# Performance work log

Hardware: AMD Instinct MI355X
Metric: run time of the kernel (lower is better)

Reference implementation:

```python
import math
import jax, jax.numpy as jnp
import numpy as np

SQRT_2_OVER_PI = 0.7978845608028654
FACIL_RATE = 2.0
FIRE_THRESH = 0.88
EPS = 1e-05

def _gelu(x):
    return 0.5 * x * (1.0 + jnp.tanh(SQRT_2_OVER_PI * (x + 0.044715 * x ** 3)))

def setup_inputs() -> dict:
    key = jax.random.key(0)
    ks = jax.random.split(key, 8)
    B, T, D, N = 4, 4096, 1024, 512
    x = jax.random.normal(ks[0], (B, T, D), jnp.float32)
    ema_x = jax.random.normal(ks[1], (D,), jnp.float32) * 0.1
    ema_x2 = ema_x ** 2 + jax.random.uniform(ks[2], (D,), jnp.float32) + 0.5
    ema_y = jax.random.normal(ks[3], (D,), jnp.float32) * 0.1
    ema_y2 = ema_y ** 2 + jax.random.uniform(ks[4], (D,), jnp.float32) + 0.5
    buf = jax.random.normal(ks[5], (N, D), jnp.float32)
    buf = buf / jnp.linalg.norm(buf, axis=-1, keepdims=True)
    facil = 1.0 + 2.0 * jax.random.uniform(ks[6], (N,), jnp.float32)  # facilitation levels >= 1
    mask = jnp.ones((N,), dtype=bool)
    return {
        'x': x,
        'log_tau_in': jnp.float32(math.log(1.0)),
        'log_tau_out': jnp.float32(math.log(1.0)),
        'log_a_in': jnp.float32(0.0),
        'log_a_out': jnp.float32(0.0),
        'log_k_boost': jnp.float32(math.log(0.5)),
        'log_k_damp': jnp.float32(math.log(0.3)),
        'ema_x': ema_x, 'ema_x2': ema_x2, 'ema_y': ema_y, 'ema_y2': ema_y2,
        'buf': buf, 'facil': facil, 'mask': mask,
    }

def reference(x, log_tau_in, log_tau_out, log_a_in, log_a_out,
              log_k_boost, log_k_damp, ema_x, ema_x2, ema_y, ema_y2,
              buf, facil, mask):
    sg = jax.lax.stop_gradient
    D = x.shape[-1]
    y = _gelu(x)
    # --- gate_211 (l1_ready steady state); z-statistics are detached in torch ---
    tau_in, tau_out = jnp.exp(log_tau_in), jnp.exp(log_tau_out)
    a_in, a_out = jax.nn.sigmoid(log_a_in), jax.nn.sigmoid(log_a_out)
    std_x = jnp.sqrt(jnp.clip(sg(ema_x2) - sg(ema_x) ** 2, 0.0)) + EPS
    z_in = jnp.mean(((sg(x) - sg(ema_x)) / std_x) ** 2, axis=-1)        # [B,T]
    std_y = jnp.sqrt(jnp.clip(sg(ema_y2) - sg(ema_y) ** 2, 0.0)) + EPS
    z_out = jnp.mean(((sg(y) - sg(ema_y)) / std_y) ** 2, axis=-1)       # [B,T]
    g_in = 1.0 - a_in + a_in * jnp.exp(-tau_in * z_in)
    g_out = 1.0 - a_out + a_out * jnp.exp(-tau_out * z_out)
    gate = g_in * g_out
    y1 = y * gate[..., None]
    # --- eval-time OCS nearest-neighbor facilitation (l2_ready, pass1_complete) ---
    k_boost = jnp.clip(jnp.exp(log_k_boost), 0.01, 4.0)
    k_damp = jnp.clip(jnp.exp(log_k_damp), 0.01, 0.9)
    y1_mean = jnp.mean(sg(y1).reshape(-1, D), axis=0)                    # [D]
    m_n = y1_mean / jnp.maximum(jnp.linalg.norm(y1_mean), 1e-12)
    buf_sg = sg(buf)
    buf_n = buf_sg / jnp.maximum(jnp.linalg.norm(buf_sg, axis=-1, keepdims=True), 1e-12)
    sims = jnp.where(mask, buf_n @ m_n, -1.0)                            # [N]
    nearest_idx = jnp.argmax(sims)
    sim_val = jnp.clip(sims[nearest_idx], 0.0, 1.0)
    fired = sim_val > FIRE_THRESH
    facil_level = sg(facil)[nearest_idx] * jnp.where(fired, FACIL_RATE, 1.0)
    v = buf_sg[nearest_idx]                                              # [D]
    valid = jnp.all(jnp.isfinite(v)) & (jnp.linalg.norm(v) >= 1e-06)
    mod = (facil_level - 1.0) * sim_val
    boost = 1.0 + sg(k_boost) * mod            # torch uses .item(): detached
    damp = jnp.maximum(0.01, 1.0 - sg(k_damp) * mod)
    proj = jnp.sum(y1 * v, axis=-1, keepdims=True)
    y_par = proj * v
    out = jnp.where(valid, y_par * boost + (y1 - y_par) * damp, y1)
    return out
```

## Files before the change

### kernel.cpp

```cpp
#include <hip/hip_runtime.h>
#include <math.h>

#define D 1024
#define NROWS 16384
#define NBUF 512

#define OFF_MEAN 0
#define OFF_KEY  1024
#define OFF_GATE 2048
#define OFF_PART 20480
#define ZERO_BYTES 4112

typedef float nfloat4 __attribute__((ext_vector_type(4)));

__device__ __forceinline__ float4 ld4(const float* p) { return *(const float4*)p; }
__device__ __forceinline__ void st4_nt(float* p, float4 v) {
    nfloat4 nv = { v.x, v.y, v.z, v.w };
    __builtin_nontemporal_store(nv, (nfloat4*)p);
}

__device__ __forceinline__ float wave_red(float v) {
    #pragma unroll
    for (int off = 32; off > 0; off >>= 1) v += __shfl_xor(v, off, 64);
    return v;
}

__device__ __forceinline__ float gelu_f(float x) {
    float u = 0.7978845608028654f * (x + 0.044715f * x * x * x);
    float e = __expf(2.0f * u);
    float t = 1.0f - 2.0f / (e + 1.0f);
    return 0.5f * x * (1.0f + t);
}

__device__ __forceinline__ float4 inv_std4(float4 m, float4 m2) {
    float4 r;
    r.x = 1.0f / (sqrtf(fmaxf(m2.x - m.x * m.x, 0.f)) + 1e-5f);
    r.y = 1.0f / (sqrtf(fmaxf(m2.y - m.y * m.y, 0.f)) + 1e-5f);
    r.z = 1.0f / (sqrtf(fmaxf(m2.z - m.z * m.z, 0.f)) + 1e-5f);
    r.w = 1.0f / (sqrtf(fmaxf(m2.w - m.w * m.w, 0.f)) + 1e-5f);
    return r;
}

template<int RPW>
__global__ __launch_bounds__(256, 4) void k_passA(const float* __restrict__ x,
                                                  const float* __restrict__ ema_x,
                                                  const float* __restrict__ ema_x2,
                                                  const float* __restrict__ ema_y,
                                                  const float* __restrict__ ema_y2,
                                                  const float* __restrict__ lti,
                                                  const float* __restrict__ lto,
                                                  const float* __restrict__ lai,
                                                  const float* __restrict__ lao,
                                                  float* __restrict__ ws) {
    __shared__ float s_acc[D];
    const int tid = threadIdx.x;
    const int wave = tid >> 6, lane = tid & 63;
    for (int i = tid; i < D; i += 256) s_acc[i] = 0.0f;
    __syncthreads();

    const float tau_in = __expf(lti[0]), tau_out = __expf(lto[0]);
    const float a_in  = 1.0f / (1.0f + __expf(-lai[0]));
    const float a_out = 1.0f / (1.0f + __expf(-lao[0]));

    int col[4];
    float4 emx[4], isx[4], emy[4], isy[4];
    #pragma unroll
    for (int j = 0; j < 4; ++j) {
        col[j] = 4 * lane + 256 * j;
        emx[j] = ld4(&ema_x[col[j]]);
        isx[j] = inv_std4(emx[j], ld4(&ema_x2[col[j]]));
        emy[j] = ld4(&ema_y[col[j]]);
        isy[j] = inv_std4(emy[j], ld4(&ema_y2[col[j]]));
    }
    float4 acc[4];
    #pragma unroll
    for (int j = 0; j < 4; ++j) acc[j] = make_float4(0.f, 0.f, 0.f, 0.f);

    const int r0 = (blockIdx.x * 4 + wave) * RPW;
    for (int r = r0; r < r0 + RPW; ++r) {
        const float* xr = x + (size_t)r * D;
        float4 yv[4];
        float zin = 0.f, zout = 0.f;
        #pragma unroll
        for (int j = 0; j < 4; ++j) {
            float4 xv = ld4(&xr[col[j]]);
            float dx, dy;
            dx = (xv.x - emx[j].x) * isx[j].x; zin += dx * dx;
            dx = (xv.y - emx[j].y) * isx[j].y; zin += dx * dx;
            dx = (xv.z - emx[j].z) * isx[j].z; zin += dx * dx;
            dx = (xv.w - emx[j].w) * isx[j].w; zin += dx * dx;
            yv[j].x = gelu_f(xv.x); dy = (yv[j].x - emy[j].x) * isy[j].x; zout += dy * dy;
            yv[j].y = gelu_f(xv.y); dy = (yv[j].y - emy[j].y) * isy[j].y; zout += dy * dy;
            yv[j].z = gelu_f(xv.z); dy = (yv[j].z - emy[j].z) * isy[j].z; zout += dy * dy;
            yv[j].w = gelu_f(xv.w); dy = (yv[j].w - emy[j].w) * isy[j].w; zout += dy * dy;
        }
        zin  = wave_red(zin)  * (1.0f / D);
        zout = wave_red(zout) * (1.0f / D);
        float g = ((1.0f - a_in)  + a_in  * __expf(-tau_in  * zin)) *
                  ((1.0f - a_out) + a_out * __expf(-tau_out * zout));
        if (lane == 0) ws[OFF_GATE + r] = g;
        #pragma unroll
        for (int j = 0; j < 4; ++j) {
            acc[j].x += yv[j].x * g;
            acc[j].y += yv[j].y * g;
            acc[j].z += yv[j].z * g;
            acc[j].w += yv[j].w * g;
        }
    }
    #pragma unroll
    for (int j = 0; j < 4; ++j) {
        atomicAdd(&s_acc[col[j] + 0], acc[j].x);
        atomicAdd(&s_acc[col[j] + 1], acc[j].y);
        atomicAdd(&s_acc[col[j] + 2], acc[j].z);
        atomicAdd(&s_acc[col[j] + 3], acc[j].w);
    }
    __syncthreads();
    float4 pv = *(float4*)&s_acc[tid * 4];
    *(float4*)&ws[OFF_PART + (size_t)blockIdx.x * D + tid * 4] = pv;
}

__global__ __launch_bounds__(256) void k_mean(float* __restrict__ ws) {
    const int tid = threadIdx.x;
    const float* P = &ws[OFF_PART + (size_t)blockIdx.x * 16 * D];
    float4 s = make_float4(0.f, 0.f, 0.f, 0.f);
    #pragma unroll
    for (int i = 0; i < 16; ++i) {
        float4 v = ld4(&P[(size_t)i * D + 4 * tid]);
        s.x += v.x; s.y += v.y; s.z += v.z; s.w += v.w;
    }
    atomicAdd(&ws[OFF_MEAN + 4 * tid + 0], s.x);
    atomicAdd(&ws[OFF_MEAN + 4 * tid + 1], s.y);
    atomicAdd(&ws[OFF_MEAN + 4 * tid + 2], s.z);
    atomicAdd(&ws[OFF_MEAN + 4 * tid + 3], s.w);
}

__global__ __launch_bounds__(256) void k_sims(const float* __restrict__ buf,
                                              const unsigned char* __restrict__ mask,
                                              float* __restrict__ ws) {
    __shared__ float s_red[4];
    __shared__ float s_inv;
    const int tid = threadIdx.x, wave = tid >> 6, lane = tid & 63;

    float4 mv = ld4(&ws[OFF_MEAN + tid * 4]);
    float ns = mv.x * mv.x + mv.y * mv.y + mv.z * mv.z + mv.w * mv.w;
    ns = wave_red(ns);
    if (lane == 0) s_red[wave] = ns;
    __syncthreads();
    if (tid == 0) {
        float t = s_red[0] + s_red[1] + s_red[2] + s_red[3];
        s_inv = 1.0f / fmaxf(sqrtf(t), 1e-12f);
    }
    __syncthreads();
    const float inv = s_inv;

    int col[4];
    float4 mvv[4];
    #pragma unroll
    for (int j = 0; j < 4; ++j) {
        col[j] = 4 * lane + 256 * j;
        mvv[j] = ld4(&ws[OFF_MEAN + col[j]]);
    }
    const int n = blockIdx.x * 4 + wave;
    const float* br = buf + (size_t)n * D;
    float dot = 0.f, bns = 0.f;
    #pragma unroll
    for (int j = 0; j < 4; ++j) {
        float4 bv = ld4(&br[col[j]]);
        dot += bv.x * mvv[j].x + bv.y * mvv[j].y + bv.z * mvv[j].z + bv.w * mvv[j].w;
        bns += bv.x * bv.x + bv.y * bv.y + bv.z * bv.z + bv.w * bv.w;
    }
    dot = wave_red(dot);
    bns = wave_red(bns);
    if (lane == 0) {
        float sim = -1.0f;
        if (mask[n]) sim = (dot * inv) / fmaxf(sqrtf(bns), 1e-12f);
        unsigned int fb = __float_as_uint(sim);
        unsigned int mono = (fb & 0x80000000u) ? ~fb : (fb | 0x80000000u);
        unsigned long long key = ((unsigned long long)mono << 32) | (unsigned int)(~n);
        atomicMax((unsigned long long*)&ws[OFF_KEY], key);
    }
}

__global__ __launch_bounds__(256, 4) void k_passB(const float* __restrict__ x,
                                                  const float* __restrict__ buf,
                                                  const float* __restrict__ facil,
                                                  const float* __restrict__ lkb,
                                                  const float* __restrict__ lkd,
                                                  const float* __restrict__ ws,
                                                  float* __restrict__ out) {
    __shared__ float s_red[4];
    __shared__ float s_sc[3];
    const int tid = threadIdx.x, wave = tid >> 6, lane = tid & 63;

    const unsigned long long key = *(const unsigned long long*)&ws[OFF_KEY];
    const int idx = (int)(~(unsigned int)(key & 0xFFFFFFFFull));
    const unsigned int mono = (unsigned int)(key >> 32);
    const unsigned int fb = (mono & 0x80000000u) ? (mono ^ 0x80000000u) : ~mono;
    const float sim = __uint_as_float(fb);

    int col[4];
    float4 vv[4];
    const float* vrow = buf + (size_t)idx * D;
    float bns = 0.f;
    #pragma unroll
    for (int j = 0; j < 4; ++j) {
        col[j] = 4 * lane + 256 * j;
        vv[j] = ld4(&vrow[col[j]]);
        if (!isfinite(vv[j].x)) bns = __uint_as_float(0x7FC00000u);
        if (!isfinite(vv[j].y)) bns = __uint_as_float(0x7FC00000u);
        if (!isfinite(vv[j].z)) bns = __uint_as_float(0x7FC00000u);
        if (!isfinite(vv[j].w)) bns = __uint_as_float(0x7FC00000u);
        bns += vv[j].x * vv[j].x + vv[j].y * vv[j].y + vv[j].z * vv[j].z + vv[j].w * vv[j].w;
    }
    bns = wave_red(bns);
    if (lane == 0) s_red[wave] = bns;
    __syncthreads();
    if (tid == 0) {
        float t = s_red[0] + s_red[1] + s_red[2] + s_red[3];
        int valid = (t >= 1e-12f) ? 1 : 0;
        float sim_val = fminf(fmaxf(sim, 0.0f), 1.0f);
        float fl = facil[idx] * ((sim_val > 0.88f) ? 2.0f : 1.0f);
        float mod = (fl - 1.0f) * sim_val;
        float kb = fminf(fmaxf(__expf(lkb[0]), 0.01f), 4.0f);
        float kd = fminf(fmaxf(__expf(lkd[0]), 0.01f), 0.9f);
        float boost = 1.0f + kb * mod;
        float damp = fmaxf(0.01f, 1.0f - kd * mod);
        s_sc[0] = valid ? damp : 1.0f;
        s_sc[1] = valid ? (boost - damp) : 0.0f;
        s_sc[2] = (float)valid;
    }
    __syncthreads();
    const float dampe = s_sc[0], coef = s_sc[1];
    if (s_sc[2] == 0.0f) {
        #pragma unroll
        for (int j = 0; j < 4; ++j) vv[j] = make_float4(0.f, 0.f, 0.f, 0.f);
    }

    const int r0 = (blockIdx.x * 4 + wave) * 2;
    for (int r = r0; r < r0 + 2; ++r) {
        const float* xr = x + (size_t)r * D;
        const float g = ws[OFF_GATE + r];
        float4 y1[4];
        float proj = 0.f;
        #pragma unroll
        for (int j = 0; j < 4; ++j) {
            float4 xv = ld4(&xr[col[j]]);
            y1[j].x = gelu_f(xv.x) * g; proj += y1[j].x * vv[j].x;
            y1[j].y = gelu_f(xv.y) * g; proj += y1[j].y * vv[j].y;
            y1[j].z = gelu_f(xv.z) * g; proj += y1[j].z * vv[j].z;
            y1[j].w = gelu_f(xv.w) * g; proj += y1[j].w * vv[j].w;
        }
        proj = wave_red(proj);
        const float pc = proj * coef;
        float* orow = out + (size_t)r * D;
        #pragma unroll
        for (int j = 0; j < 4; ++j) {
            float4 o;
            o.x = y1[j].x * dampe + pc * vv[j].x;
            o.y = y1[j].y * dampe + pc * vv[j].y;
            o.z = y1[j].z * dampe + pc * vv[j].z;
            o.w = y1[j].w * dampe + pc * vv[j].w;
            st4_nt(&orow[col[j]], o);
        }
    }
}

extern "C" void kernel_launch(void* const* d_in, const int* in_sizes, int n_in,
                              void* d_out, int out_size, void* d_ws, size_t ws_size,
                              hipStream_t stream) {
    const float* x      = (const float*)d_in[0];
    const float* lti    = (const float*)d_in[1];
    const float* lto    = (const float*)d_in[2];
    const float* lai    = (const float*)d_in[3];
    const float* lao    = (const float*)d_in[4];
    const float* lkb    = (const float*)d_in[5];
    const float* lkd    = (const float*)d_in[6];
    const float* ema_x  = (const float*)d_in[7];
    const float* ema_x2 = (const float*)d_in[8];
    const float* ema_y  = (const float*)d_in[9];
    const float* ema_y2 = (const float*)d_in[10];
    const float* buf    = (const float*)d_in[11];
    const float* facil  = (const float*)d_in[12];
    const unsigned char* mask = (const unsigned char*)d_in[13];
    float* ws  = (float*)d_ws;
    float* out = (float*)d_out;

    int NP;
    if      (ws_size >= ((size_t)OFF_PART + 2048u * D) * 4) NP = 2048;
    else if (ws_size >= ((size_t)OFF_PART + 1024u * D) * 4) NP = 1024;
    else                                                    NP = 512;

    (void)hipMemsetAsync(d_ws, 0, ZERO_BYTES, stream);
    if (NP == 2048)
        hipLaunchKernelGGL(k_passA<2>, dim3(2048), dim3(256), 0, stream,
                           x, ema_x, ema_x2, ema_y, ema_y2, lti, lto, lai, lao, ws);
    else if (NP == 1024)
        hipLaunchKernelGGL(k_passA<4>, dim3(1024), dim3(256), 0, stream,
                           x, ema_x, ema_x2, ema_y, ema_y2, lti, lto, lai, lao, ws);
    else
        hipLaunchKernelGGL(k_passA<8>, dim3(512), dim3(256), 0, stream,
                           x, ema_x, ema_x2, ema_y, ema_y2, lti, lto, lai, lao, ws);
    hipLaunchKernelGGL(k_mean,  dim3(NP / 16), dim3(256), 0, stream, ws);
    hipLaunchKernelGGL(k_sims,  dim3(128), dim3(256), 0, stream, buf, mask, ws);
    hipLaunchKernelGGL(k_passB, dim3(2048), dim3(256), 0, stream,
                       x, buf, facil, lkb, lkd, ws, out);
}
```

Baseline: 217.8 us.

## Process two rows per iteration, fold stats into LDS, cheaper GELU, fewer blocks

Several changes land together. GELU is rewritten algebraically as x - x/(1+exp(2u)) using a hardware reciprocal. The EMA statistics are precomputed per block into shared memory as a scale and an offset so the z-scores become FMAs. Both passes now handle two rows per iteration with all loads issued up front, and each wave covers 8 rows. Grids are fixed at 512 blocks for pass A and pass B, dropping the workspace-size-dependent partial count. The aim is more memory-level parallelism and less ALU work, at the cost of more registers and fewer blocks in flight.

```diff
diff --git a/kernel.cpp b/kernel.cpp
--- a/kernel.cpp
+++ b/kernel.cpp
@@ -4,6 +4,7 @@
 #define D 1024
 #define NROWS 16384
 #define NBUF 512
+#define NBLKA 512
 
 #define OFF_MEAN 0
 #define OFF_KEY  1024
@@ -26,22 +27,20 @@
 }
 
 __device__ __forceinline__ float gelu_f(float x) {
-    float u = 0.7978845608028654f * (x + 0.044715f * x * x * x);
-    float e = __expf(2.0f * u);
-    float t = 1.0f - 2.0f / (e + 1.0f);
-    return 0.5f * x * (1.0f + t);
-}
-
-__device__ __forceinline__ float4 inv_std4(float4 m, float4 m2) {
-    float4 r;
-    r.x = 1.0f / (sqrtf(fmaxf(m2.x - m.x * m.x, 0.f)) + 1e-5f);
-    r.y = 1.0f / (sqrtf(fmaxf(m2.y - m.y * m.y, 0.f)) + 1e-5f);
-    r.z = 1.0f / (sqrtf(fmaxf(m2.z - m.z * m.z, 0.f)) + 1e-5f);
-    r.w = 1.0f / (sqrtf(fmaxf(m2.w - m.w * m.w, 0.f)) + 1e-5f);
-    return r;
-}
-
-template<int RPW>
+    float x2 = x * x;
+    float t1 = fmaf(0.044715f, x2, 1.0f);
+    float u2 = (1.5957691216057308f * x) * t1;
+    float e  = __expf(u2);
+    float r  = __builtin_amdgcn_rcpf(e + 1.0f);
+    return fmaf(-x, r, x);
+}
+
+__device__ __forceinline__ float4 gelu4(float4 x) {
+    float4 y;
+    y.x = gelu_f(x.x); y.y = gelu_f(x.y); y.z = gelu_f(x.z); y.w = gelu_f(x.w);
+    return y;
+}
+
 __global__ __launch_bounds__(256, 4) void k_passA(const float* __restrict__ x,
                                                   const float* __restrict__ ema_x,
                                                   const float* __restrict__ ema_x2,
@@ -52,10 +51,23 @@
                                                   const float* __restrict__ lai,
                                                   const float* __restrict__ lao,
                                                   float* __restrict__ ws) {
+    __shared__ float s_stat[4096];
     __shared__ float s_acc[D];
-    const int tid = threadIdx.x;
-    const int wave = tid >> 6, lane = tid & 63;
-    for (int i = tid; i < D; i += 256) s_acc[i] = 0.0f;
+    const int tid = threadIdx.x, wave = tid >> 6, lane = tid & 63;
+
+    for (int i = tid; i < 1024; i += 256) {
+        float mx = ema_x[i];
+        float vx = fmaxf(ema_x2[i] - mx * mx, 0.0f);
+        float ax = 1.0f / (sqrtf(vx) + 1e-5f);
+        s_stat[i]        = ax;
+        s_stat[1024 + i] = mx * ax;
+        float my = ema_y[i];
+        float vy = fmaxf(ema_y2[i] - my * my, 0.0f);
+        float ay = 1.0f / (sqrtf(vy) + 1e-5f);
+        s_stat[2048 + i] = ay;
+        s_stat[3072 + i] = my * ay;
+        s_acc[i] = 0.0f;
+    }
     __syncthreads();
 
     const float tau_in = __expf(lti[0]), tau_out = __expf(lto[0]);
@@ -63,48 +75,66 @@
     const float a_out = 1.0f / (1.0f + __expf(-lao[0]));
 
     int col[4];
-    float4 emx[4], isx[4], emy[4], isy[4];
-    #pragma unroll
-    for (int j = 0; j < 4; ++j) {
-        col[j] = 4 * lane + 256 * j;
-        emx[j] = ld4(&ema_x[col[j]]);
-        isx[j] = inv_std4(emx[j], ld4(&ema_x2[col[j]]));
-        emy[j] = ld4(&ema_y[col[j]]);
-        isy[j] = inv_std4(emy[j], ld4(&ema_y2[col[j]]));
-    }
+    #pragma unroll
+    for (int j = 0; j < 4; ++j) col[j] = 4 * lane + 256 * j;
+
     float4 acc[4];
     #pragma unroll
     for (int j = 0; j < 4; ++j) acc[j] = make_float4(0.f, 0.f, 0.f, 0.f);
 
-    const int r0 = (blockIdx.x * 4 + wave) * RPW;
-    for (int r = r0; r < r0 + RPW; ++r) {
-        const float* xr = x + (size_t)r * D;
-        float4 yv[4];
-        float zin = 0.f, zout = 0.f;
+    const int r0 = (blockIdx.x * 4 + wave) * 8;
+    #pragma unroll
+    for (int k = 0; k < 4; ++k) {
+        const int rA = r0 + 2 * k, rB = rA + 1;
+        const float* pA = x + (size_t)rA * D;
+        const float* pB = x + (size_t)rB * D;
+        float4 xA[4], xB[4];
+        #pragma unroll
+        for (int j = 0; j < 4; ++j) { xA[j] = ld4(&pA[col[j]]); xB[j] = ld4(&pB[col[j]]); }
+
+        float4 yA[4], yB[4];
+        float zinA = 0.f, zinB = 0.f, zoutA = 0.f, zoutB = 0.f;
         #pragma unroll
         for (int j = 0; j < 4; ++j) {
-            float4 xv = ld4(&xr[col[j]]);
-            float dx, dy;
-            dx = (xv.x - emx[j].x) * isx[j].x; zin += dx * dx;
-            dx = (xv.y - emx[j].y) * isx[j].y; zin += dx * dx;
-            dx = (xv.z - emx[j].z) * isx[j].z; zin += dx * dx;
-            dx = (xv.w - emx[j].w) * isx[j].w; zin += dx * dx;
-            yv[j].x = gelu_f(xv.x); dy = (yv[j].x - emy[j].x) * isy[j].x; zout += dy * dy;
-            yv[j].y = gelu_f(xv.y); dy = (yv[j].y - emy[j].y) * isy[j].y; zout += dy * dy;
-            yv[j].z = gelu_f(xv.z); dy = (yv[j].z - emy[j].z) * isy[j].z; zout += dy * dy;
-            yv[j].w = gelu_f(xv.w); dy = (yv[j].w - emy[j].w) * isy[j].w; zout += dy * dy;
+            float4 a  = *(const float4*)&s_stat[col[j]];
+            float4 bb = *(const float4*)&s_stat[1024 + col[j]];
+            float d;
+            d = fmaf(xA[j].x, a.x, -bb.x); zinA = fmaf(d, d, zinA);
+            d = fmaf(xA[j].y, a.y, -bb.y); zinA = fmaf(d, d, zinA);
+            d = fmaf(xA[j].z, a.z, -bb.z); zinA = fmaf(d, d, zinA);
+            d = fmaf(xA[j].w, a.w, -bb.w); zinA = fmaf(d, d, zinA);
+            d = fmaf(xB[j].x, a.x, -bb.x); zinB = fmaf(d, d, zinB);
+            d = fmaf(xB[j].y, a.y, -bb.y); zinB = fmaf(d, d, zinB);
+            d = fmaf(xB[j].z, a.z, -bb.z); zinB = fmaf(d, d, zinB);
+            d = fmaf(xB[j].w, a.w, -bb.w); zinB = fmaf(d, d, zinB);
+            yA[j] = gelu4(xA[j]);
+            yB[j] = gelu4(xB[j]);
+            float4 ay = *(const float4*)&s_stat[2048 + col[j]];
+            float4 by = *(const float4*)&s_stat[3072 + col[j]];
+            d = fmaf(yA[j].x, ay.x, -by.x); zoutA = fmaf(d, d, zoutA);
+            d = fmaf(yA[j].y, ay.y, -by.y); zoutA = fmaf(d, d, zoutA);
+            d = fmaf(yA[j].z, ay.z, -by.z); zoutA = fmaf(d, d, zoutA);
+            d = fmaf(yA[j].w, ay.w, -by.w); zoutA = fmaf(d, d, zoutA);
+            d = fmaf(yB[j].x, ay.x, -by.x); zoutB = fmaf(d, d, zoutB);
+            d = fmaf(yB[j].y, ay.y, -by.y); zoutB = fmaf(d, d, zoutB);
+            d = fmaf(yB[j].z, ay.z, -by.z); zoutB = fmaf(d, d, zoutB);
+            d = fmaf(yB[j].w, ay.w, -by.w); zoutB = fmaf(d, d, zoutB);
         }
-        zin  = wave_red(zin)  * (1.0f / D);
-        zout = wave_red(zout) * (1.0f / D);
-        float g = ((1.0f - a_in)  + a_in  * __expf(-tau_in  * zin)) *
-                  ((1.0f - a_out) + a_out * __expf(-tau_out * zout));
-        if (lane == 0) ws[OFF_GATE + r] = g;
+        zinA  = wave_red(zinA)  * (1.0f / D);
+        zinB  = wave_red(zinB)  * (1.0f / D);
+        zoutA = wave_red(zoutA) * (1.0f / D);
+        zoutB = wave_red(zoutB) * (1.0f / D);
+        float gA = ((1.0f - a_in)  + a_in  * __expf(-tau_in  * zinA)) *
+                   ((1.0f - a_out) + a_out * __expf(-tau_out * zoutA));
+        float gB = ((1.0f - a_in)  + a_in  * __expf(-tau_in  * zinB)) *
+                   ((1.0f - a_out) + a_out * __expf(-tau_out * zoutB));
+        if (lane == 0) { ws[OFF_GATE + rA] = gA; ws[OFF_GATE + rB] = gB; }
         #pragma unroll
         for (int j = 0; j < 4; ++j) {
-            acc[j].x += yv[j].x * g;
-            acc[j].y += yv[j].y * g;
-            acc[j].z += yv[j].z * g;
-            acc[j].w += yv[j].w * g;
+            acc[j].x = fmaf(yA[j].x, gA, fmaf(yB[j].x, gB, acc[j].x));
+            acc[j].y = fmaf(yA[j].y, gA, fmaf(yB[j].y, gB, acc[j].y));
+            acc[j].z = fmaf(yA[j].z, gA, fmaf(yB[j].z, gB, acc[j].z));
+            acc[j].w = fmaf(yA[j].w, gA, fmaf(yB[j].w, gB, acc[j].w));
         }
     }
     #pragma unroll
@@ -115,8 +145,7 @@
         atomicAdd(&s_acc[col[j] + 3], acc[j].w);
     }
     __syncthreads();
-    float4 pv = *(float4*)&s_acc[tid * 4];
-    *(float4*)&ws[OFF_PART + (size_t)blockIdx.x * D + tid * 4] = pv;
+    *(float4*)&ws[OFF_PART + (size_t)blockIdx.x * D + 4 * tid] = *(float4*)&s_acc[4 * tid];
 }
 
 __global__ __launch_bounds__(256) void k_mean(float* __restrict__ ws) {
@@ -141,7 +170,7 @@
     __shared__ float s_inv;
     const int tid = threadIdx.x, wave = tid >> 6, lane = tid & 63;
 
-    float4 mv = ld4(&ws[OFF_MEAN + tid * 4]);
+    float4 mv = ld4(&ws[OFF_MEAN + 4 * tid]);
     float ns = mv.x * mv.x + mv.y * mv.y + mv.z * mv.z + mv.w * mv.w;
     ns = wave_red(ns);
     if (lane == 0) s_red[wave] = ns;
@@ -166,8 +195,10 @@
     #pragma unroll
     for (int j = 0; j < 4; ++j) {
         float4 bv = ld4(&br[col[j]]);
-        dot += bv.x * mvv[j].x + bv.y * mvv[j].y + bv.z * mvv[j].z + bv.w * mvv[j].w;
-        bns += bv.x * bv.x + bv.y * bv.y + bv.z * bv.z + bv.w * bv.w;
+        dot = fmaf(bv.x, mvv[j].x, dot); dot = fmaf(bv.y, mvv[j].y, dot);
+        dot = fmaf(bv.z, mvv[j].z, dot); dot = fmaf(bv.w, mvv[j].w, dot);
+        bns = fmaf(bv.x, bv.x, bns); bns = fmaf(bv.y, bv.y, bns);
+        bns = fmaf(bv.z, bv.z, bns); bns = fmaf(bv.w, bv.w, bns);
     }
     dot = wave_red(dot);
     bns = wave_red(bns);
@@ -188,6 +219,7 @@
                                                   const float* __restrict__ lkd,
                                                   const float* __restrict__ ws,
                                                   float* __restrict__ out) {
+    __shared__ float s_v[D];
     __shared__ float s_red[4];
     __shared__ float s_sc[3];
     const int tid = threadIdx.x, wave = tid >> 6, lane = tid & 63;
@@ -198,20 +230,11 @@
     const unsigned int fb = (mono & 0x80000000u) ? (mono ^ 0x80000000u) : ~mono;
     const float sim = __uint_as_float(fb);
 
-    int col[4];
-    float4 vv[4];
-    const float* vrow = buf + (size_t)idx * D;
+    float4 vt = ld4(&buf[(size_t)idx * D + 4 * tid]);
     float bns = 0.f;
-    #pragma unroll
-    for (int j = 0; j < 4; ++j) {
-        col[j] = 4 * lane + 256 * j;
-        vv[j] = ld4(&vrow[col[j]]);
-        if (!isfinite(vv[j].x)) bns = __uint_as_float(0x7FC00000u);
-        if (!isfinite(vv[j].y)) bns = __uint_as_float(0x7FC00000u);
-        if (!isfinite(vv[j].z)) bns = __uint_as_float(0x7FC00000u);
-        if (!isfinite(vv[j].w)) bns = __uint_as_float(0x7FC00000u);
-        bns += vv[j].x * vv[j].x + vv[j].y * vv[j].y + vv[j].z * vv[j].z + vv[j].w * vv[j].w;
-    }
+    if (!isfinite(vt.x) || !isfinite(vt.y) || !isfinite(vt.z) || !isfinite(vt.w))
+        bns = __uint_as_float(0x7FC00000u);
+    bns += vt.x * vt.x + vt.y * vt.y + vt.z * vt.z + vt.w * vt.w;
     bns = wave_red(bns);
     if (lane == 0) s_red[wave] = bns;
     __syncthreads();
@@ -231,36 +254,59 @@
     }
     __syncthreads();
     const float dampe = s_sc[0], coef = s_sc[1];
-    if (s_sc[2] == 0.0f) {
-        #pragma unroll
-        for (int j = 0; j < 4; ++j) vv[j] = make_float4(0.f, 0.f, 0.f, 0.f);
-    }
-
-    const int r0 = (blockIdx.x * 4 + wave) * 2;
-    for (int r = r0; r < r0 + 2; ++r) {
-        const float* xr = x + (size_t)r * D;
-        const float g = ws[OFF_GATE + r];
-        float4 y1[4];
-        float proj = 0.f;
+    if (s_sc[2] == 0.0f) vt = make_float4(0.f, 0.f, 0.f, 0.f);
+    *(float4*)&s_v[4 * tid] = vt;
+    __syncthreads();
+
+    int col[4];
+    float4 vv[4];
+    #pragma unroll
+    for (int j = 0; j < 4; ++j) {
+        col[j] = 4 * lane + 256 * j;
+        vv[j] = *(const float4*)&s_v[col[j]];
+    }
+
+    const int r0 = (blockIdx.x * 4 + wave) * 8;
+    #pragma unroll
+    for (int k = 0; k < 4; ++k) {
+        const int rA = r0 + 2 * k, rB = rA + 1;
+        const float gA = ws[OFF_GATE + rA], gB = ws[OFF_GATE + rB];
+        const float* pA = x + (size_t)rA * D;
+        const float* pB = x + (size_t)rB * D;
+        float4 xA[4], xB[4];
+        #pragma unroll
+        for (int j = 0; j < 4; ++j) { xA[j] = ld4(&pA[col[j]]); xB[j] = ld4(&pB[col[j]]); }
+        float4 yA[4], yB[4];
+        float projA = 0.f, projB = 0.f;
         #pragma unroll
         for (int j = 0; j < 4; ++j) {
-            float4 xv = ld4(&xr[col[j]]);
-            y1[j].x = gelu_f(xv.x) * g; proj += y1[j].x * vv[j].x;
-            y1[j].y = gelu_f(xv.y) * g; proj += y1[j].y * vv[j].y;
-            y1[j].z = gelu_f(xv.z) * g; proj += y1[j].z * vv[j].z;
-            y1[j].w = gelu_f(xv.w) * g; proj += y1[j].w * vv[j].w;
+            yA[j] = gelu4(xA[j]);
+            yA[j].x *= gA; yA[j].y *= gA; yA[j].z *= gA; yA[j].w *= gA;
+            yB[j] = gelu4(xB[j]);
+            yB[j].x *= gB; yB[j].y *= gB; yB[j].z *= gB; yB[j].w *= gB;
+            projA = fmaf(yA[j].x, vv[j].x, projA); projA = fmaf(yA[j].y, vv[j].y, projA);
+            projA = fmaf(yA[j].z, vv[j].z, projA); projA = fmaf(yA[j].w, vv[j].w, projA);
+            projB = fmaf(yB[j].x, vv[j].x, projB); projB = fmaf(yB[j].y, vv[j].y, projB);
+            projB = fmaf(yB[j].z, vv[j].z, projB); projB = fmaf(yB[j].w, vv[j].w, projB);
         }
-        proj = wave_red(proj);
-        const float pc = proj * coef;
-        float* orow = out + (size_t)r * D;
+        projA = wave_red(projA);
+        projB = wave_red(projB);
+        const float pcA = projA * coef, pcB = projB * coef;
+        float* oA = out + (size_t)rA * D;
+        float* oB = out + (size_t)rB * D;
         #pragma unroll
         for (int j = 0; j < 4; ++j) {
             float4 o;
-            o.x = y1[j].x * dampe + pc * vv[j].x;
-            o.y = y1[j].y * dampe + pc * vv[j].y;
-            o.z = y1[j].z * dampe + pc * vv[j].z;
-            o.w = y1[j].w * dampe + pc * vv[j].w;
-            st4_nt(&orow[col[j]], o);
+            o.x = fmaf(yA[j].x, dampe, pcA * vv[j].x);
+            o.y = fmaf(yA[j].y, dampe, pcA * vv[j].y);
+            o.z = fmaf(yA[j].z, dampe, pcA * vv[j].z);
+            o.w = fmaf(yA[j].w, dampe, pcA * vv[j].w);
+            st4_nt(&oA[col[j]], o);
+            o.x = fmaf(yB[j].x, dampe, pcB * vv[j].x);
+            o.y = fmaf(yB[j].y, dampe, pcB * vv[j].y);
+            o.z = fmaf(yB[j].z, dampe, pcB * vv[j].z);
+            o.w = fmaf(yB[j].w, dampe, pcB * vv[j].w);
+            st4_nt(&oB[col[j]], o);
         }
     }
 }
@@ -285,23 +331,11 @@
     float* ws  = (float*)d_ws;
     float* out = (float*)d_out;
 
-    int NP;
-    if      (ws_size >= ((size_t)OFF_PART + 2048u * D) * 4) NP = 2048;
-    else if (ws_size >= ((size_t)OFF_PART + 1024u * D) * 4) NP = 1024;
-    else                                                    NP = 512;
-
     (void)hipMemsetAsync(d_ws, 0, ZERO_BYTES, stream);
-    if (NP == 2048)
-        hipLaunchKernelGGL(k_passA<2>, dim3(2048), dim3(256), 0, stream,
-                           x, ema_x, ema_x2, ema_y, ema_y2, lti, lto, lai, lao, ws);
-    else if (NP == 1024)
-        hipLaunchKernelGGL(k_passA<4>, dim3(1024), dim3(256), 0, stream,
-                           x, ema_x, ema_x2, ema_y, ema_y2, lti, lto, lai, lao, ws);
-    else
-        hipLaunchKernelGGL(k_passA<8>, dim3(512), dim3(256), 0, stream,
-                           x, ema_x, ema_x2, ema_y, ema_y2, lti, lto, lai, lao, ws);
-    hipLaunchKernelGGL(k_mean,  dim3(NP / 16), dim3(256), 0, stream, ws);
+    hipLaunchKernelGGL(k_passA, dim3(NBLKA), dim3(256), 0, stream,
+                       x, ema_x, ema_x2, ema_y, ema_y2, lti, lto, lai, lao, ws);
+    hipLaunchKernelGGL(k_mean,  dim3(NBLKA / 16), dim3(256), 0, stream, ws);
     hipLaunchKernelGGL(k_sims,  dim3(128), dim3(256), 0, stream, buf, mask, ws);
-    hipLaunchKernelGGL(k_passB, dim3(2048), dim3(256), 0, stream,
+    hipLaunchKernelGGL(k_passB, dim3(NBLKA), dim3(256), 0, stream,
                        x, buf, facil, lkb, lkd, ws, out);
 }
```

Result: faster. 190.6 us (-12.5%).
